# Kernel tuning notes

Measured on AMD Instinct MI355X. Metric: run time of the kernel, lower is better.

The kernel has to match this reference:

```python
import jax, jax.numpy as jnp
import numpy as np

N_NODES = 50000


def _mean_aggregate(x, src, dst):
    # gather source features along edges, segment-mean into destinations
    msg = x[src]                                             # [E, d] irregular gather
    agg = jax.ops.segment_sum(msg, dst, num_segments=N_NODES)  # [N, d]
    deg = jax.ops.segment_sum(jnp.ones((src.shape[0],), x.dtype), dst,
                              num_segments=N_NODES)
    return agg / jnp.maximum(deg, 1.0)[:, None]


def setup_inputs() -> dict:
    key = jax.random.key(0)
    ks = jax.random.split(key, 8)
    d_in, d_hid, d_out, L, E = 128, 128, 40, 3, 800000
    s = 1.0 / np.sqrt(d_hid)
    return {
        "x": jax.random.normal(ks[0], (N_NODES, d_in), jnp.float32),
        "edge_index": jax.random.randint(ks[1], (2, E), 0, N_NODES, jnp.int64),
        "Wl": jax.random.normal(ks[2], (L, d_hid, d_hid), jnp.float32) * s,
        "Wr": jax.random.normal(ks[3], (L, d_hid, d_hid), jnp.float32) * s,
        "bl": jnp.zeros((L, d_hid), jnp.float32),
        "W1": jax.random.normal(ks[4], (L * d_hid, d_hid), jnp.float32) * s,
        "b1": jnp.zeros((d_hid,), jnp.float32),
        "W2": jax.random.normal(ks[5], (d_hid, d_out), jnp.float32) * s,
        "b2": jnp.zeros((d_out,), jnp.float32),
    }


def reference(x, edge_index, Wl, Wr, bl, W1, b1, W2, b2):
    src, dst = edge_index[0], edge_index[1]
    h = x
    outs = []
    for i in range(Wl.shape[0]):  # num_layers (structurally small loop)
        m = _mean_aggregate(h, src, dst)          # mean_j x_j  [N, d]
        h = m @ Wl[i] + bl[i] + h @ Wr[i]         # SAGEConv: lin_l(aggr) + lin_r(x)
        outs.append(h)
    z = jnp.concatenate(outs, axis=1)             # [N, L*d]
    z = jax.nn.relu(z @ W1 + b1)
    z = z @ W2 + b2
    return jax.nn.log_softmax(z, axis=1)
```

## Files before the change

kernel.cpp:

```cpp
#include <hip/hip_runtime.h>
#include <math.h>

#define N_NODES 50000
#define D 128
#define LAYERS 3
#define DZ 384
#define DOUT 40
#define BUCKETS 196
#define BR 32
#define ADJ_LDS 2048

typedef __attribute__((ext_vector_type(4))) float f32x4;
typedef __attribute__((ext_vector_type(8))) short short8;

static __device__ __forceinline__ unsigned short f2bf(float f) {
    unsigned int u = __float_as_uint(f);
    u += 0x7FFFu + ((u >> 16) & 1u);
    return (unsigned short)(u >> 16);
}
static __device__ __forceinline__ float bflo(unsigned int u) {
    return __uint_as_float(u << 16);
}
static __device__ __forceinline__ float bfhi(unsigned int u) {
    return __uint_as_float(u & 0xFFFF0000u);
}
static __device__ __forceinline__ void accq(float* acc, uint4 q, float wgt) {
    acc[0] = fmaf(wgt, bflo(q.x), acc[0]);
    acc[1] = fmaf(wgt, bfhi(q.x), acc[1]);
    acc[2] = fmaf(wgt, bflo(q.y), acc[2]);
    acc[3] = fmaf(wgt, bfhi(q.y), acc[3]);
    acc[4] = fmaf(wgt, bflo(q.z), acc[4]);
    acc[5] = fmaf(wgt, bfhi(q.z), acc[5]);
    acc[6] = fmaf(wgt, bflo(q.w), acc[6]);
    acc[7] = fmaf(wgt, bfhi(q.w), acc[7]);
}


__global__ __launch_bounds__(256) void hist1_kernel(const int* __restrict__ dst, int E, int CH,
                                                    int nblk1, int* __restrict__ H) {
    __shared__ int h[BUCKETS];
    int t = threadIdx.x;
    if (t < BUCKETS) h[t] = 0;
    __syncthreads();
    int s = blockIdx.x * CH, e = min(E, s + CH);
    for (int i = s + t; i < e; i += 256) atomicAdd(&h[dst[i] >> 8], 1);
    __syncthreads();
    if (t < BUCKETS) H[t * nblk1 + blockIdx.x] = h[t];
}

__global__ __launch_bounds__(512) void scanS_kernel(int* __restrict__ H, int nblk1,
                                                    int* __restrict__ T) {
    __shared__ int s[512];
    int t = threadIdx.x, k = blockIdx.x;
    int v = (t < nblk1) ? H[k * nblk1 + t] : 0;
    s[t] = v;
    __syncthreads();
    for (int off = 1; off < 512; off <<= 1) {
        int u = (t >= off) ? s[t - off] : 0;
        __syncthreads();
        s[t] += u;
        __syncthreads();
    }
    if (t < nblk1) H[k * nblk1 + t] = s[t] - v;
    if (t == 511) T[k] = s[511];
}

__global__ __launch_bounds__(256) void bstart_kernel(const int* __restrict__ T,
                                                     int* __restrict__ bucketStart,
                                                     int* __restrict__ offs, int E) {
    __shared__ int s[256];
    int t = threadIdx.x;
    int v = (t < BUCKETS) ? T[t] : 0;
    s[t] = v;
    __syncthreads();
    for (int off = 1; off < 256; off <<= 1) {
        int u = (t >= off) ? s[t - off] : 0;
        __syncthreads();
        s[t] += u;
        __syncthreads();
    }
    if (t < BUCKETS) bucketStart[t] = s[t] - v;
    if (t == 0) { bucketStart[BUCKETS] = E; offs[N_NODES] = E; }
}

__global__ __launch_bounds__(256) void scatter_kernel(const int* __restrict__ src,
                                                      const int* __restrict__ dst, int E, int CH,
                                                      int nblk1, const int* __restrict__ H,
                                                      const int* __restrict__ bucketStart,
                                                      unsigned int* __restrict__ recs) {
    __shared__ int cur[BUCKETS];
    int t = threadIdx.x;
    if (t < BUCKETS) cur[t] = bucketStart[t] + H[t * nblk1 + blockIdx.x];
    __syncthreads();
    int s = blockIdx.x * CH, e = min(E, s + CH);
    for (int i = s + t; i < e; i += 256) {
        int d = dst[i];
        int pos = atomicAdd(&cur[d >> 8], 1);
        recs[pos] = (unsigned int)(src[i] & 0xFFFF) | ((unsigned int)(d & 255) << 16);
    }
}

__global__ __launch_bounds__(256) void bucket_csr_kernel(const unsigned int* __restrict__ recs,
                                                         const int* __restrict__ bucketStart,
                                                         int* __restrict__ offs,
                                                         unsigned short* __restrict__ adj) {
    __shared__ int h[256];
    __shared__ int sc[256];
    __shared__ int cur[256];
    int t = threadIdx.x, k = blockIdx.x;
    int bs = bucketStart[k], be = bucketStart[k + 1];
    h[t] = 0;
    __syncthreads();
    for (int i = bs + t; i < be; i += 256) atomicAdd(&h[(recs[i] >> 16) & 255], 1);
    __syncthreads();
    int v = h[t];
    sc[t] = v;
    __syncthreads();
    for (int off = 1; off < 256; off <<= 1) {
        int u = (t >= off) ? sc[t - off] : 0;
        __syncthreads();
        sc[t] += u;
        __syncthreads();
    }
    int excl = sc[t] - v;
    int node = k * 256 + t;
    if (node < N_NODES) offs[node] = bs + excl;
    cur[t] = bs + excl;
    __syncthreads();
    for (int i = bs + t; i < be; i += 256) {
        unsigned int r = recs[i];
        int pos = atomicAdd(&cur[(r >> 16) & 255], 1);
        adj[pos] = (unsigned short)(r & 0xFFFF);
    }
}


__global__ __launch_bounds__(256) void prep_kernel(const float* __restrict__ x,
                                                   const float* __restrict__ Wl,
                                                   const float* __restrict__ Wr,
                                                   const float* __restrict__ W1,
                                                   const float* __restrict__ W2,
                                                   unsigned short* __restrict__ xb,
                                                   unsigned short* __restrict__ WT,
                                                   unsigned short* __restrict__ W1T,
                                                   unsigned short* __restrict__ W2T,
                                                   int n4) {
    int i = blockIdx.x * blockDim.x + threadIdx.x;
    if (i < n4) {
        const float4 v = ((const float4*)x)[i];
        unsigned int lo = ((unsigned int)f2bf(v.y) << 16) | f2bf(v.x);
        unsigned int hi = ((unsigned int)f2bf(v.w) << 16) | f2bf(v.z);
        ((unsigned int*)xb)[i * 2] = lo;
        ((unsigned int*)xb)[i * 2 + 1] = hi;
        return;
    }
    int j = i - n4;
    if (j < LAYERS * 128 * 256) {
        int layer = j >> 15;
        int r = j & 32767;
        int c = r >> 8, k = r & 255;
        const float* W = (k < 128) ? (Wl + layer * 16384) : (Wr + layer * 16384);
        WT[j] = f2bf(W[(k & 127) * 128 + c]);
        return;
    }
    j -= LAYERS * 128 * 256;
    if (j < 128 * 384) {
        int c = j / 384, k = j - c * 384;
        W1T[j] = f2bf(W1[k * 128 + c]);
        return;
    }
    j -= 128 * 384;
    if (j < 48 * 128) {
        int c = j >> 7, k = j & 127;
        W2T[j] = (c < DOUT) ? f2bf(W2[k * DOUT + c]) : (unsigned short)0;
    }
}

__global__ __launch_bounds__(512) void sage_fused_kernel(
        const unsigned short* __restrict__ h,
        const int* __restrict__ offs, const unsigned short* __restrict__ adj,
        const unsigned short* __restrict__ WT,
        const float* __restrict__ bl,
        unsigned short* __restrict__ zout) {
    __shared__ unsigned short mlds[BR][136];
    __shared__ unsigned short hlds[BR][136];
    __shared__ unsigned short adjlds[ADJ_LDS];
    int tid = threadIdx.x;
    int r0 = blockIdx.x * BR;
    int gid = tid >> 4, l16 = tid & 15;

    {
        int row = tid >> 4, c8 = (tid & 15) * 8;
        int rc = min(r0 + row, N_NODES - 1);
        *(uint4*)(&hlds[row][c8]) = *(const uint4*)(h + (size_t)rc * D + c8);
    }
    int segS = offs[min(r0, N_NODES)];
    int segE = offs[min(r0 + BR, N_NODES)];
    int stage = min(segE - segS, ADJ_LDS);
    for (int i = tid; i < stage; i += 512) adjlds[i] = adj[segS + i];
    __syncthreads();

    {
        const unsigned short* hb = h + l16 * 8;
        int node = r0 + gid;
        float acc[8];
#pragma unroll
        for (int j = 0; j < 8; ++j) acc[j] = 0.f;
        int s = 0, e = 0;
        if (node < N_NODES) { s = offs[node]; e = offs[node + 1]; }
        for (int k = s; k < e; k += 8) {
            int e1 = e - 1;
            int a[8];
#pragma unroll
            for (int j = 0; j < 8; ++j) {
                int kk = min(k + j, e1);
                int rr = kk - segS;
                a[j] = (rr < stage) ? (int)adjlds[rr] : (int)adj[kk];
            }
            uint4 q[8];
#pragma unroll
            for (int j = 0; j < 8; ++j) q[j] = *(const uint4*)(hb + (size_t)a[j] * D);
            accq(acc, q[0], 1.f);
#pragma unroll
            for (int j = 1; j < 8; ++j) {
                float w = (k + j < e) ? 1.f : 0.f;
                accq(acc, q[j], w);
            }
        }
        float inv = 1.f / fmaxf((float)(e - s), 1.f);
        uint4 o;
        o.x = ((unsigned int)f2bf(acc[1] * inv) << 16) | f2bf(acc[0] * inv);
        o.y = ((unsigned int)f2bf(acc[3] * inv) << 16) | f2bf(acc[2] * inv);
        o.z = ((unsigned int)f2bf(acc[5] * inv) << 16) | f2bf(acc[4] * inv);
        o.w = ((unsigned int)f2bf(acc[7] * inv) << 16) | f2bf(acc[6] * inv);
        *(uint4*)(&mlds[gid][l16 * 8]) = o;
    }
    __syncthreads();

    int wid = tid >> 6;
    int lane = tid & 63;
    int lrow = lane & 15;
    int lk8 = (lane >> 4) * 8;
    int colBase = wid * 16;
    f32x4 acc0 = (f32x4){0.f,0.f,0.f,0.f};
    f32x4 acc1 = (f32x4){0.f,0.f,0.f,0.f};

#pragma unroll
    for (int kc = 0; kc < 8; ++kc) {
        short8 aF0, aF1;
        if (kc < 4) {
            aF0 = *(const short8*)(&mlds[lrow][kc * 32 + lk8]);
            aF1 = *(const short8*)(&mlds[16 + lrow][kc * 32 + lk8]);
        } else {
            aF0 = *(const short8*)(&hlds[lrow][(kc - 4) * 32 + lk8]);
            aF1 = *(const short8*)(&hlds[16 + lrow][(kc - 4) * 32 + lk8]);
        }
        short8 bF = *(const short8*)(WT + (size_t)(colBase + lrow) * 256 + kc * 32 + lk8);
        acc0 = __builtin_amdgcn_mfma_f32_16x16x32_bf16(aF0, bF, acc0, 0, 0, 0);
        acc1 = __builtin_amdgcn_mfma_f32_16x16x32_bf16(aF1, bF, acc1, 0, 0, 0);
    }

    int ocol = lane & 15;
    int orow0 = r0 + (lane >> 4) * 4;
    int col = colBase + ocol;
    float b = bl[col];
#pragma unroll
    for (int j = 0; j < 4; ++j) {
        int ra = orow0 + j;
        int rb = ra + 16;
        if (ra < N_NODES) zout[(size_t)ra * D + col] = f2bf(acc0[j] + b);
        if (rb < N_NODES) zout[(size_t)rb * D + col] = f2bf(acc1[j] + b);
    }
}

__global__ __launch_bounds__(512) void mlp_fused_kernel(
        const unsigned short* __restrict__ z0,
        const unsigned short* __restrict__ z1b,
        const unsigned short* __restrict__ z2,
        const unsigned short* __restrict__ W1T,
        const float* __restrict__ b1,
        const unsigned short* __restrict__ W2T,
        const float* __restrict__ b2,
        float* __restrict__ out) {
    __shared__ unsigned short zs[BR][392];
    int tid = threadIdx.x;
    int wid = tid >> 6;
    int lane = tid & 63;
    int r0 = blockIdx.x * BR;
    int lrow = lane & 15;
    int lk8 = (lane >> 4) * 8;
    int colBase = wid * 16;

    short8 bw[12];
#pragma unroll
    for (int kc = 0; kc < 12; ++kc) {
        bw[kc] = *(const short8*)(W1T + (size_t)(colBase + lrow) * DZ + kc * 32 + lk8);
    }

    const unsigned short* zbuf[3] = {z0, z1b, z2};
#pragma unroll
    for (int b = 0; b < 3; ++b) {
        int row = tid >> 4, c8 = (tid & 15) * 8;
        int rc = min(r0 + row, N_NODES - 1);
        *(uint4*)(&zs[row][b * 128 + c8]) = *(const uint4*)(zbuf[b] + (size_t)rc * D + c8);
    }
    __syncthreads();

    f32x4 acc0 = (f32x4){0.f,0.f,0.f,0.f};
    f32x4 acc1 = (f32x4){0.f,0.f,0.f,0.f};
#pragma unroll
    for (int kc = 0; kc < 12; ++kc) {
        short8 aF0 = *(const short8*)(&zs[lrow][kc * 32 + lk8]);
        short8 aF1 = *(const short8*)(&zs[16 + lrow][kc * 32 + lk8]);
        acc0 = __builtin_amdgcn_mfma_f32_16x16x32_bf16(aF0, bw[kc], acc0, 0, 0, 0);
        acc1 = __builtin_amdgcn_mfma_f32_16x16x32_bf16(aF1, bw[kc], acc1, 0, 0, 0);
    }
    __syncthreads();

    int ocol = lane & 15;
    int lrow0 = (lane >> 4) * 4;
    {
        int col = colBase + ocol;
        float b = b1[col];
#pragma unroll
        for (int j = 0; j < 4; ++j) {
            zs[lrow0 + j][col] = f2bf(fmaxf(acc0[j] + b, 0.f));
            zs[16 + lrow0 + j][col] = f2bf(fmaxf(acc1[j] + b, 0.f));
        }
    }
    __syncthreads();

    if (wid < 2) {
        f32x4 acc[3];
#pragma unroll
        for (int t = 0; t < 3; ++t) acc[t] = (f32x4){0.f,0.f,0.f,0.f};
        int lr = wid * 16 + lrow;
#pragma unroll
        for (int kc = 0; kc < 4; ++kc) {
            short8 aF = *(const short8*)(&zs[lr][kc * 32 + lk8]);
#pragma unroll
            for (int ct = 0; ct < 3; ++ct) {
                short8 bF = *(const short8*)(W2T + (size_t)(ct * 16 + lrow) * 128 + kc * 32 + lk8);
                acc[ct] = __builtin_amdgcn_mfma_f32_16x16x32_bf16(aF, bF, acc[ct], 0, 0, 0);
            }
        }

        float b0 = b2[ocol];
        float b1v = b2[16 + ocol];
        float b2v = (ocol < 8) ? b2[32 + ocol] : 0.f;

#pragma unroll
        for (int j = 0; j < 4; ++j) {
            int orow = r0 + wid * 16 + (lane >> 4) * 4 + j;
            float v0 = acc[0][j] + b0;
            float v1 = acc[1][j] + b1v;
            float v2 = (ocol < 8) ? (acc[2][j] + b2v) : -1e30f;
            float mx = fmaxf(fmaxf(v0, v1), v2);
            mx = fmaxf(mx, __shfl_xor(mx, 1));
            mx = fmaxf(mx, __shfl_xor(mx, 2));
            mx = fmaxf(mx, __shfl_xor(mx, 4));
            mx = fmaxf(mx, __shfl_xor(mx, 8));
            float es = expf(v0 - mx) + expf(v1 - mx) + ((ocol < 8) ? expf(v2 - mx) : 0.f);
            es += __shfl_xor(es, 1);
            es += __shfl_xor(es, 2);
            es += __shfl_xor(es, 4);
            es += __shfl_xor(es, 8);
            float ls = logf(es);
            if (orow < N_NODES) {
                out[(size_t)orow * DOUT + ocol] = v0 - mx - ls;
                out[(size_t)orow * DOUT + 16 + ocol] = v1 - mx - ls;
                if (ocol < 8) out[(size_t)orow * DOUT + 32 + ocol] = v2 - mx - ls;
            }
        }
    }
}


extern "C" void kernel_launch(void* const* d_in, const int* in_sizes, int n_in,
                              void* d_out, int out_size, void* d_ws, size_t ws_size,
                              hipStream_t stream) {
    const float* x   = (const float*)d_in[0];
    const int*   ei  = (const int*)d_in[1];
    const float* Wl  = (const float*)d_in[2];
    const float* Wr  = (const float*)d_in[3];
    const float* bl  = (const float*)d_in[4];
    const float* W1  = (const float*)d_in[5];
    const float* b1  = (const float*)d_in[6];
    const float* W2  = (const float*)d_in[7];
    const float* b2  = (const float*)d_in[8];
    float* out = (float*)d_out;

    const int E = in_sizes[1] / 2;
    const int* src = ei;
    const int* dst = ei + E;

    int CH = 2048;
    int nblk1 = (E + CH - 1) / CH;
    if (nblk1 > 512) { CH = ((E + 511) / 512 + 255) & ~255; nblk1 = (E + CH - 1) / CH; }

    char* p = (char*)d_ws;
    auto take = [&p](size_t bytes) { char* q = p; p += (bytes + 255) & ~(size_t)255; return q; };
    int* offs        = (int*)take((N_NODES + 1) * sizeof(int));
    int* H           = (int*)take((size_t)BUCKETS * nblk1 * sizeof(int));
    int* T           = (int*)take(BUCKETS * sizeof(int));
    int* bucketStart = (int*)take((BUCKETS + 1) * sizeof(int));
    unsigned int*   recs = (unsigned int*)take((size_t)E * sizeof(unsigned int));
    unsigned short* adj  = (unsigned short*)take((size_t)E * sizeof(unsigned short));
    unsigned short* xb  = (unsigned short*)take((size_t)N_NODES * D * 2);
    unsigned short* z0  = (unsigned short*)take((size_t)N_NODES * D * 2);
    unsigned short* z1  = (unsigned short*)take((size_t)N_NODES * D * 2);
    unsigned short* z2  = (unsigned short*)take((size_t)N_NODES * D * 2);
    unsigned short* WT  = (unsigned short*)take((size_t)LAYERS * 128 * 256 * 2);
    unsigned short* W1T = (unsigned short*)take((size_t)128 * 384 * 2);
    unsigned short* W2T = (unsigned short*)take((size_t)48 * 128 * 2);

    int n4 = N_NODES * D / 4;
    int prep_total = n4 + LAYERS * 128 * 256 + 128 * 384 + 48 * 128;
    prep_kernel<<<(prep_total + 255) / 256, 256, 0, stream>>>(
        x, Wl, Wr, W1, W2, xb, WT, W1T, W2T, n4);

    hist1_kernel<<<nblk1, 256, 0, stream>>>(dst, E, CH, nblk1, H);
    scanS_kernel<<<BUCKETS, 512, 0, stream>>>(H, nblk1, T);
    bstart_kernel<<<1, 256, 0, stream>>>(T, bucketStart, offs, E);
    scatter_kernel<<<nblk1, 256, 0, stream>>>(src, dst, E, CH, nblk1, H, bucketStart, recs);
    bucket_csr_kernel<<<BUCKETS, 256, 0, stream>>>(recs, bucketStart, offs, adj);

    int fgrid = (N_NODES + BR - 1) / BR;

    unsigned short* zsb[3] = {z0, z1, z2};
    for (int i = 0; i < LAYERS; ++i) {
        const unsigned short* hin = (i == 0) ? xb : zsb[i - 1];
        sage_fused_kernel<<<fgrid, 512, 0, stream>>>(
            hin, offs, adj, WT + (size_t)i * 128 * 256, bl + (size_t)i * D, zsb[i]);
    }

    mlp_fused_kernel<<<fgrid, 512, 0, stream>>>(z0, z1, z2, W1T, b1, W2T, b2, out);
}
```

Before: 198.0 us.

## Balance neighbor aggregation by splitting block edge range evenly across groups

Replaces the one-group-per-node gather with an even split of the block's whole edge segment across the 32 thread groups. Each group walks node boundaries and flushes partial sums into an fp32 LDS accumulator with shared-memory atomics. The goal is to remove load imbalance from varying node degrees and the wasted padded lanes in short neighbor lists. In exchange it adds LDS atomics, a serial boundary search, about 17KB more LDS per block (which may lower occupancy), and an extra barrier.

```diff
diff --git a/kernel.cpp b/kernel.cpp
--- a/kernel.cpp
+++ b/kernel.cpp
@@ -185,6 +185,8 @@
     __shared__ unsigned short mlds[BR][136];
     __shared__ unsigned short hlds[BR][136];
     __shared__ unsigned short adjlds[ADJ_LDS];
+    __shared__ float macc[BR][132];
+    __shared__ int offsl[BR + 1];
     int tid = threadIdx.x;
     int r0 = blockIdx.x * BR;
     int gid = tid >> 4, l16 = tid & 15;
@@ -194,46 +196,82 @@
         int rc = min(r0 + row, N_NODES - 1);
         *(uint4*)(&hlds[row][c8]) = *(const uint4*)(h + (size_t)rc * D + c8);
     }
-    int segS = offs[min(r0, N_NODES)];
-    int segE = offs[min(r0 + BR, N_NODES)];
-    int stage = min(segE - segS, ADJ_LDS);
-    for (int i = tid; i < stage; i += 512) adjlds[i] = adj[segS + i];
+    if (tid <= BR) offsl[tid] = offs[min(r0 + tid, N_NODES)];
+    {
+        float* mf = &macc[0][0];
+        for (int i = tid; i < BR * 132; i += 512) mf[i] = 0.f;
+    }
+    __syncthreads();
+    int segS = offsl[0];
+    int segLen = offsl[BR] - segS;
+    int staged = min(segLen, ADJ_LDS);
+    for (int i = tid; i < staged; i += 512) adjlds[i] = adj[segS + i];
     __syncthreads();
 
     {
         const unsigned short* hb = h + l16 * 8;
-        int node = r0 + gid;
-        float acc[8];
-#pragma unroll
-        for (int j = 0; j < 8; ++j) acc[j] = 0.f;
-        int s = 0, e = 0;
-        if (node < N_NODES) { s = offs[node]; e = offs[node + 1]; }
-        for (int k = s; k < e; k += 8) {
-            int e1 = e - 1;
-            int a[8];
-#pragma unroll
-            for (int j = 0; j < 8; ++j) {
-                int kk = min(k + j, e1);
-                int rr = kk - segS;
-                a[j] = (rr < stage) ? (int)adjlds[rr] : (int)adj[kk];
+        int chunk = (segLen + BR - 1) / BR;
+        int c0 = gid * chunk;
+        int c1 = min(c0 + chunk, segLen);
+        if (c0 < c1) {
+            int node = 0;
+            while (node < BR - 1 && offsl[node + 1] - segS <= c0) node++;
+            int bnd = offsl[node + 1] - segS;
+            float acc[8];
+#pragma unroll
+            for (int j = 0; j < 8; ++j) acc[j] = 0.f;
+            bool dirty = false;
+
+            for (int k = c0; k < c1; k += 8) {
+                int a[8];
+#pragma unroll
+                for (int j = 0; j < 8; ++j) {
+                    int kk = min(k + j, c1 - 1);
+                    a[j] = (kk < staged) ? (int)adjlds[kk] : (int)adj[segS + kk];
+                }
+                uint4 q[8];
+#pragma unroll
+                for (int j = 0; j < 8; ++j) q[j] = *(const uint4*)(hb + (size_t)a[j] * D);
+#pragma unroll
+                for (int j = 0; j < 8; ++j) {
+                    int kj = k + j;
+                    if (kj < c1) {
+                        while (kj >= bnd) {
+                            if (dirty) {
+#pragma unroll
+                                for (int jj = 0; jj < 8; ++jj) {
+                                    atomicAdd(&macc[node][l16 * 8 + jj], acc[jj]);
+                                    acc[jj] = 0.f;
+                                }
+                                dirty = false;
+                            }
+                            node++;
+                            bnd = offsl[node + 1] - segS;
+                        }
+                        accq(acc, q[j], 1.f);
+                        dirty = true;
+                    }
+                }
             }
-            uint4 q[8];
-#pragma unroll
-            for (int j = 0; j < 8; ++j) q[j] = *(const uint4*)(hb + (size_t)a[j] * D);
-            accq(acc, q[0], 1.f);
-#pragma unroll
-            for (int j = 1; j < 8; ++j) {
-                float w = (k + j < e) ? 1.f : 0.f;
-                accq(acc, q[j], w);
+            if (dirty) {
+#pragma unroll
+                for (int jj = 0; jj < 8; ++jj)
+                    atomicAdd(&macc[node][l16 * 8 + jj], acc[jj]);
             }
         }
-        float inv = 1.f / fmaxf((float)(e - s), 1.f);
+    }
+    __syncthreads();
+
+    {
+        int row = tid >> 4, c8 = (tid & 15) * 8;
+        int deg = offsl[row + 1] - offsl[row];
+        float inv = 1.f / fmaxf((float)deg, 1.f);
         uint4 o;
-        o.x = ((unsigned int)f2bf(acc[1] * inv) << 16) | f2bf(acc[0] * inv);
-        o.y = ((unsigned int)f2bf(acc[3] * inv) << 16) | f2bf(acc[2] * inv);
-        o.z = ((unsigned int)f2bf(acc[5] * inv) << 16) | f2bf(acc[4] * inv);
-        o.w = ((unsigned int)f2bf(acc[7] * inv) << 16) | f2bf(acc[6] * inv);
-        *(uint4*)(&mlds[gid][l16 * 8]) = o;
+        o.x = ((unsigned int)f2bf(macc[row][c8 + 1] * inv) << 16) | f2bf(macc[row][c8 + 0] * inv);
+        o.y = ((unsigned int)f2bf(macc[row][c8 + 3] * inv) << 16) | f2bf(macc[row][c8 + 2] * inv);
+        o.z = ((unsigned int)f2bf(macc[row][c8 + 5] * inv) << 16) | f2bf(macc[row][c8 + 4] * inv);
+        o.w = ((unsigned int)f2bf(macc[row][c8 + 7] * inv) << 16) | f2bf(macc[row][c8 + 6] * inv);
+        *(uint4*)(&mlds[row][c8]) = o;
     }
     __syncthreads();
 
```

Measured after the change: 334.9 us. +69.2%, slower.

## Process nodes in degree-sorted order to balance per-block gather work

Applied to the files above, without the earlier changes.

Adds a counting sort of nodes by descending in-degree, built from four new kernels, and makes the SAGE and MLP kernels handle rows through this permutation. Each 32-row block then holds nodes of similar degree, which is meant to cut divergence and tail imbalance in the neighbour-gather loop. The cost is extra sort kernels and scattered row loads and stores through perm. The LDS staging of adjacency indices is also dropped, since a block's edge ranges are no longer contiguous.

```diff
diff --git a/kernel.cpp b/kernel.cpp
--- a/kernel.cpp
+++ b/kernel.cpp
@@ -8,7 +8,6 @@
 #define DOUT 40
 #define BUCKETS 196
 #define BR 32
-#define ADJ_LDS 2048
 
 typedef __attribute__((ext_vector_type(4))) float f32x4;
 typedef __attribute__((ext_vector_type(8))) short short8;
@@ -131,6 +130,56 @@
         unsigned int r = recs[i];
         int pos = atomicAdd(&cur[(r >> 16) & 255], 1);
         adj[pos] = (unsigned short)(r & 0xFFFF);
+    }
+}
+
+
+__global__ __launch_bounds__(256) void deg_hist_kernel(const int* __restrict__ offs,
+                                                       int* __restrict__ HP) {
+    __shared__ int h[256];
+    int t = threadIdx.x;
+    h[t] = 0;
+    __syncthreads();
+    int n = blockIdx.x * 256 + t;
+    if (n < N_NODES) {
+        int deg = offs[n + 1] - offs[n];
+        int key = 255 - min(deg, 255);
+        atomicAdd(&h[key], 1);
+    }
+    __syncthreads();
+    HP[t * BUCKETS + blockIdx.x] = h[t];
+}
+
+__global__ __launch_bounds__(256) void bstart256_kernel(const int* __restrict__ T,
+                                                        int* __restrict__ binStart) {
+    __shared__ int s[256];
+    int t = threadIdx.x;
+    int v = T[t];
+    s[t] = v;
+    __syncthreads();
+    for (int off = 1; off < 256; off <<= 1) {
+        int u = (t >= off) ? s[t - off] : 0;
+        __syncthreads();
+        s[t] += u;
+        __syncthreads();
+    }
+    binStart[t] = s[t] - v;
+}
+
+__global__ __launch_bounds__(256) void deg_scatter_kernel(const int* __restrict__ offs,
+                                                          const int* __restrict__ HP,
+                                                          const int* __restrict__ binStart,
+                                                          int* __restrict__ perm) {
+    __shared__ int cur[256];
+    int t = threadIdx.x;
+    cur[t] = binStart[t] + HP[t * BUCKETS + blockIdx.x];
+    __syncthreads();
+    int n = blockIdx.x * 256 + t;
+    if (n < N_NODES) {
+        int deg = offs[n + 1] - offs[n];
+        int key = 255 - min(deg, 255);
+        int pos = atomicAdd(&cur[key], 1);
+        perm[pos] = n;
     }
 }
 
@@ -179,44 +228,37 @@
 __global__ __launch_bounds__(512) void sage_fused_kernel(
         const unsigned short* __restrict__ h,
         const int* __restrict__ offs, const unsigned short* __restrict__ adj,
+        const int* __restrict__ perm,
         const unsigned short* __restrict__ WT,
         const float* __restrict__ bl,
         unsigned short* __restrict__ zout) {
     __shared__ unsigned short mlds[BR][136];
     __shared__ unsigned short hlds[BR][136];
-    __shared__ unsigned short adjlds[ADJ_LDS];
+    __shared__ int perml[BR];
     int tid = threadIdx.x;
     int r0 = blockIdx.x * BR;
     int gid = tid >> 4, l16 = tid & 15;
 
+    if (tid < BR) perml[tid] = perm[min(r0 + tid, N_NODES - 1)];
+    __syncthreads();
+
     {
         int row = tid >> 4, c8 = (tid & 15) * 8;
-        int rc = min(r0 + row, N_NODES - 1);
-        *(uint4*)(&hlds[row][c8]) = *(const uint4*)(h + (size_t)rc * D + c8);
-    }
-    int segS = offs[min(r0, N_NODES)];
-    int segE = offs[min(r0 + BR, N_NODES)];
-    int stage = min(segE - segS, ADJ_LDS);
-    for (int i = tid; i < stage; i += 512) adjlds[i] = adj[segS + i];
-    __syncthreads();
+        *(uint4*)(&hlds[row][c8]) = *(const uint4*)(h + (size_t)perml[row] * D + c8);
+    }
 
     {
         const unsigned short* hb = h + l16 * 8;
-        int node = r0 + gid;
+        int node = perml[gid];
         float acc[8];
 #pragma unroll
         for (int j = 0; j < 8; ++j) acc[j] = 0.f;
-        int s = 0, e = 0;
-        if (node < N_NODES) { s = offs[node]; e = offs[node + 1]; }
+        int s = offs[node], e = offs[node + 1];
         for (int k = s; k < e; k += 8) {
             int e1 = e - 1;
             int a[8];
 #pragma unroll
-            for (int j = 0; j < 8; ++j) {
-                int kk = min(k + j, e1);
-                int rr = kk - segS;
-                a[j] = (rr < stage) ? (int)adjlds[rr] : (int)adj[kk];
-            }
+            for (int j = 0; j < 8; ++j) a[j] = adj[min(k + j, e1)];
             uint4 q[8];
 #pragma unroll
             for (int j = 0; j < 8; ++j) q[j] = *(const uint4*)(hb + (size_t)a[j] * D);
@@ -261,15 +303,15 @@
     }
 
     int ocol = lane & 15;
-    int orow0 = r0 + (lane >> 4) * 4;
+    int tr0 = (lane >> 4) * 4;
     int col = colBase + ocol;
     float b = bl[col];
 #pragma unroll
     for (int j = 0; j < 4; ++j) {
-        int ra = orow0 + j;
-        int rb = ra + 16;
-        if (ra < N_NODES) zout[(size_t)ra * D + col] = f2bf(acc0[j] + b);
-        if (rb < N_NODES) zout[(size_t)rb * D + col] = f2bf(acc1[j] + b);
+        int ra = perml[tr0 + j];
+        int rb = perml[tr0 + 16 + j];
+        zout[(size_t)ra * D + col] = f2bf(acc0[j] + b);
+        zout[(size_t)rb * D + col] = f2bf(acc1[j] + b);
     }
 }
 
@@ -277,12 +319,14 @@
         const unsigned short* __restrict__ z0,
         const unsigned short* __restrict__ z1b,
         const unsigned short* __restrict__ z2,
+        const int* __restrict__ perm,
         const unsigned short* __restrict__ W1T,
         const float* __restrict__ b1,
         const unsigned short* __restrict__ W2T,
         const float* __restrict__ b2,
         float* __restrict__ out) {
     __shared__ unsigned short zs[BR][392];
+    __shared__ int perml[BR];
     int tid = threadIdx.x;
     int wid = tid >> 6;
     int lane = tid & 63;
@@ -291,18 +335,20 @@
     int lk8 = (lane >> 4) * 8;
     int colBase = wid * 16;
 
+    if (tid < BR) perml[tid] = perm[min(r0 + tid, N_NODES - 1)];
+
     short8 bw[12];
 #pragma unroll
     for (int kc = 0; kc < 12; ++kc) {
         bw[kc] = *(const short8*)(W1T + (size_t)(colBase + lrow) * DZ + kc * 32 + lk8);
     }
+    __syncthreads();
 
     const unsigned short* zbuf[3] = {z0, z1b, z2};
 #pragma unroll
     for (int b = 0; b < 3; ++b) {
         int row = tid >> 4, c8 = (tid & 15) * 8;
-        int rc = min(r0 + row, N_NODES - 1);
-        *(uint4*)(&zs[row][b * 128 + c8]) = *(const uint4*)(zbuf[b] + (size_t)rc * D + c8);
+        *(uint4*)(&zs[row][b * 128 + c8]) = *(const uint4*)(zbuf[b] + (size_t)perml[row] * D + c8);
     }
     __syncthreads();
 
@@ -351,7 +397,8 @@
 
 #pragma unroll
         for (int j = 0; j < 4; ++j) {
-            int orow = r0 + wid * 16 + (lane >> 4) * 4 + j;
+            int tr = wid * 16 + (lane >> 4) * 4 + j;
+            int orow = perml[tr];
             float v0 = acc[0][j] + b0;
             float v1 = acc[1][j] + b1v;
             float v2 = (ocol < 8) ? (acc[2][j] + b2v) : -1e30f;
@@ -366,11 +413,9 @@
             es += __shfl_xor(es, 4);
             es += __shfl_xor(es, 8);
             float ls = logf(es);
-            if (orow < N_NODES) {
-                out[(size_t)orow * DOUT + ocol] = v0 - mx - ls;
-                out[(size_t)orow * DOUT + 16 + ocol] = v1 - mx - ls;
-                if (ocol < 8) out[(size_t)orow * DOUT + 32 + ocol] = v2 - mx - ls;
-            }
+            out[(size_t)orow * DOUT + ocol] = v0 - mx - ls;
+            out[(size_t)orow * DOUT + 16 + ocol] = v1 - mx - ls;
+            if (ocol < 8) out[(size_t)orow * DOUT + 32 + ocol] = v2 - mx - ls;
         }
     }
 }
@@ -406,6 +451,10 @@
     int* bucketStart = (int*)take((BUCKETS + 1) * sizeof(int));
     unsigned int*   recs = (unsigned int*)take((size_t)E * sizeof(unsigned int));
     unsigned short* adj  = (unsigned short*)take((size_t)E * sizeof(unsigned short));
+    int* HP          = (int*)take((size_t)256 * BUCKETS * sizeof(int));
+    int* TP          = (int*)take(256 * sizeof(int));
+    int* binStart    = (int*)take(256 * sizeof(int));
+    int* perm        = (int*)take((size_t)N_NODES * sizeof(int));
     unsigned short* xb  = (unsigned short*)take((size_t)N_NODES * D * 2);
     unsigned short* z0  = (unsigned short*)take((size_t)N_NODES * D * 2);
     unsigned short* z1  = (unsigned short*)take((size_t)N_NODES * D * 2);
@@ -425,14 +474,19 @@
     scatter_kernel<<<nblk1, 256, 0, stream>>>(src, dst, E, CH, nblk1, H, bucketStart, recs);
     bucket_csr_kernel<<<BUCKETS, 256, 0, stream>>>(recs, bucketStart, offs, adj);
 
+    deg_hist_kernel<<<BUCKETS, 256, 0, stream>>>(offs, HP);
+    scanS_kernel<<<256, 512, 0, stream>>>(HP, BUCKETS, TP);
+    bstart256_kernel<<<1, 256, 0, stream>>>(TP, binStart);
+    deg_scatter_kernel<<<BUCKETS, 256, 0, stream>>>(offs, HP, binStart, perm);
+
     int fgrid = (N_NODES + BR - 1) / BR;
 
     unsigned short* zsb[3] = {z0, z1, z2};
     for (int i = 0; i < LAYERS; ++i) {
         const unsigned short* hin = (i == 0) ? xb : zsb[i - 1];
         sage_fused_kernel<<<fgrid, 512, 0, stream>>>(
-            hin, offs, adj, WT + (size_t)i * 128 * 256, bl + (size_t)i * D, zsb[i]);
-    }
-
-    mlp_fused_kernel<<<fgrid, 512, 0, stream>>>(z0, z1, z2, W1T, b1, W2T, b2, out);
-}
+            hin, offs, adj, perm, WT + (size_t)i * 128 * 256, bl + (size_t)i * D, zsb[i]);
+    }
+
+    mlp_fused_kernel<<<fgrid, 512, 0, stream>>>(z0, z1, z2, perm, W1T, b1, W2T, b2, out);
+}
```

Result: faster. 191.9 us (-3.1%).
